# Kernel tuning notes

Measured on AMD Instinct MI355X. Metric: run time of the kernel, lower is better.

The kernel has to match this reference:

```python
import jax, jax.numpy as jnp
import numpy as np

B, S, D = 4, 4096, 256

def setup_inputs() -> dict:
    key = jax.random.key(0)
    kx, kq, kk, kv = jax.random.split(key, 4)
    # torch nn.Linear(D, D) weight init: U(-1/sqrt(D), 1/sqrt(D)), stored as [out, in]
    bound = 1.0 / np.sqrt(D)
    x = jax.random.normal(kx, (B, S, D), dtype=jnp.float32)
    Wq = jax.random.uniform(kq, (D, D), dtype=jnp.float32, minval=-bound, maxval=bound)
    Wk = jax.random.uniform(kk, (D, D), dtype=jnp.float32, minval=-bound, maxval=bound)
    Wv = jax.random.uniform(kv, (D, D), dtype=jnp.float32, minval=-bound, maxval=bound)
    return {"x": x, "Wq": Wq, "Wk": Wk, "Wv": Wv}

def reference(x, Wq, Wk, Wv):
    # Linear with weight [out,in]: y = x @ W^T
    Q = jnp.einsum('bsd,ed->bse', x, Wq)
    K = jnp.einsum('bsd,ed->bse', x, Wk)
    V = jnp.einsum('bsd,ed->bse', x, Wv)
    d = x.shape[-1]
    scores = jnp.einsum('bqe,bke->bqk', Q, K) / jnp.sqrt(jnp.float32(d))  # [B,S,S]
    S_len = x.shape[1]
    causal = jnp.tril(jnp.ones((S_len, S_len), dtype=bool))
    scores = jnp.where(causal, scores, -jnp.inf)
    attn = jax.nn.softmax(scores, axis=-1)
    return jnp.einsum('bqk,bke->bqe', attn, V)
```

## Files before the change

### kernel.cpp

```cpp
#include <hip/hip_runtime.h>

typedef unsigned short u16;
typedef unsigned int u32;
typedef __attribute__((ext_vector_type(8))) short bf16x8;
typedef __attribute__((ext_vector_type(4))) float f32x4;
typedef __attribute__((ext_vector_type(16))) float f32x16;
typedef __attribute__((ext_vector_type(2))) unsigned int u32x2;

#define MFMA16 __builtin_amdgcn_mfma_f32_16x16x32_bf16
#define MFMA32 __builtin_amdgcn_mfma_f32_32x32x16_bf16

__device__ __forceinline__ u16 f2bf(float f) {
  u32 u = __builtin_bit_cast(u32, f);
  u = u + 0x7FFFu + ((u >> 16) & 1u);
  return (u16)(u >> 16);
}
__device__ __forceinline__ u32 pk2(float lo, float hi) {
  return (u32)f2bf(lo) | ((u32)f2bf(hi) << 16);
}
__device__ __forceinline__ float bf2f(u32 x) {
  return __builtin_bit_cast(float, x << 16);
}
__device__ __forceinline__ u32 cvtpk(float lo, float hi) {
  u32 r;
  asm("v_cvt_pk_bf16_f32 %0, %1, %2" : "=v"(r) : "v"(lo), "v"(hi));
  return r;
}
__device__ __forceinline__ void pswap(u32& x, u32& y) {
  asm("v_permlane32_swap_b32 %0, %1" : "+v"(x), "+v"(y));
}
__device__ __forceinline__ void gld16(const void* gp, void* lp) {
  __builtin_amdgcn_global_load_lds((const __attribute__((address_space(1))) u32*)gp,
                                   (__attribute__((address_space(3))) u32*)lp, 16, 0, 0);
}

__global__ __launch_bounds__(256) void cvt_kernel(
    const float* __restrict__ x, const float* __restrict__ wq,
    const float* __restrict__ wk, const float* __restrict__ wv,
    u16* __restrict__ xbf, u16* __restrict__ wbf) {
  int idx = blockIdx.x * 256 + threadIdx.x;
  if (idx < 1048576) {
    float4 v = ((const float4*)x)[idx];
    uint2 u; u.x = pk2(v.x, v.y); u.y = pk2(v.z, v.w);
    ((uint2*)xbf)[idx] = u;
  } else {
    int j = idx - 1048576;
    const float* W = (j < 16384) ? wq : (j < 32768) ? wk : wv;
    int k = j & 16383;
    float4 v = ((const float4*)W)[k];
    uint2 u; u.x = pk2(v.x, v.y); u.y = pk2(v.z, v.w);
    ((uint2*)wbf)[j] = u;
  }
}

__global__ __launch_bounds__(256, 2) void proj_kernel(
    const u16* __restrict__ xbf, const u16* __restrict__ wbf,
    u16* __restrict__ Qs, u16* __restrict__ Ks, u16* __restrict__ Vt) {
  int tile = blockIdx.x, mat = blockIdx.y;
  int tid = threadIdx.x, w = tid >> 6, lane = tid & 63, b15 = lane & 15, g = lane >> 4;
  int base = tile * 64 + w * 16;
  const u16* W = wbf + mat * 65536;
  const u16* Xp = xbf + (size_t)(base + b15) * 256;
  f32x4 acc[16] = {};
  if (mat < 2) {
#pragma unroll
    for (int kk = 0; kk < 8; ++kk) {
      bf16x8 xf = *(const bf16x8*)(Xp + kk * 32 + g * 8);
#pragma unroll
      for (int eb = 0; eb < 16; ++eb) {
        bf16x8 wf = *(const bf16x8*)(W + (size_t)(eb * 16 + b15) * 256 + kk * 32 + g * 8);
        acc[eb] = MFMA16(xf, wf, acc[eb], 0, 0, 0);
      }
    }
    float scale = (mat == 0) ? 0.0901684400555602f : 1.0f;
    u16* dst = (mat == 0) ? Qs : Ks;
#pragma unroll
    for (int eb = 0; eb < 16; ++eb)
#pragma unroll
      for (int r = 0; r < 4; ++r)
        dst[(size_t)(base + g * 4 + r) * 256 + eb * 16 + b15] = f2bf(acc[eb][r] * scale);
  } else {
#pragma unroll
    for (int kk = 0; kk < 8; ++kk) {
      bf16x8 xf = *(const bf16x8*)(Xp + kk * 32 + g * 8);
#pragma unroll
      for (int eb = 0; eb < 16; ++eb) {
        bf16x8 wf = *(const bf16x8*)(W + (size_t)(eb * 16 + b15) * 256 + kk * 32 + g * 8);
        acc[eb] = MFMA16(wf, xf, acc[eb], 0, 0, 0);
      }
    }
    int sglob = base + b15;
    int b = sglob >> 12, sl = sglob & 4095;
#pragma unroll
    for (int eb = 0; eb < 16; ++eb)
#pragma unroll
      for (int r = 0; r < 4; ++r) {
        int e = eb * 16 + g * 4 + r;
        Vt[((size_t)(b * 256 + e) << 12) + sl] = f2bf(acc[eb][r]);
      }
  }
}

__global__ __launch_bounds__(256, 2) void attn_kernel(
    const u16* __restrict__ Qs, const u16* __restrict__ Ks_,
    const u16* __restrict__ Vt_, u16* __restrict__ pacc, float2* __restrict__ pml) {
  __shared__ u16 Kd[2][8192];
  __shared__ u16 Vd[2][8192];

  int bid = blockIdx.x;
  int xcd = bid & 7;
  int b = xcd >> 1;
  int j = ((bid >> 3) << 1) | (bid & 1);
  int t0, c0, t1 = -1, c1 = 0;
  if (j < 16) {
    int g = j & 7;
    if (j < 8) { t0 = 4 * g;     t1 = 4 * g + 3; }
    else       { t0 = 4 * g + 1; t1 = 4 * g + 2; }
    c0 = g; c1 = g;
  } else {
    int jj = j - 16;
    int g = 1;
#pragma unroll
    for (int gg = 2; gg <= 7; ++gg) if (jj >= 2 * gg * (gg - 1)) g = gg;
    int r = jj - 2 * g * (g - 1);
    t0 = 4 * g + r / g; c0 = r % g;
  }

  int tid = threadIdx.x, w = tid >> 6, lane = tid & 63;
  int l31 = lane & 31, h = lane >> 5;

  int Koff[4], Voff[4];
#pragma unroll
  for (int i = 0; i < 4; ++i) {
    int o = (w * 4 + i) * 1024 + lane * 16;
    int row = o >> 9;
    Koff[i] = row * 512 + ((o & 511) ^ ((row & 15) << 4));
    int e = o >> 6;
    Voff[i] = e * 8192 + ((o & 63) ^ (((e >> 1) & 3) << 4));
  }
  const char* Kgb = (const char*)(Ks_ + (size_t)b * 4096 * 256);
  const char* Vgb = (const char*)(Vt_ + (size_t)b * 1048576);
  char* KL = (char*)&Kd[0][0];
  char* VL = (char*)&Vd[0][0];

  auto stage = [&](int buf, int kt) {
    size_t kb = (size_t)kt * 32 * 512;
    size_t vb = (size_t)kt * 64;
#pragma unroll
    for (int i = 0; i < 4; ++i)
      gld16(Kgb + kb + Koff[i], KL + buf * 16384 + (w * 4 + i) * 1024);
#pragma unroll
    for (int i = 0; i < 4; ++i)
      gld16(Vgb + vb + Voff[i], VL + buf * 16384 + (w * 4 + i) * 1024);
  };

  auto process = [&](int tt, int c) {
    int g4 = tt >> 2;
    int uid = b * 144 + 2 * g4 * (g4 + 1) + (tt & 3) * (g4 + 1) + c;
    int qbase = tt * 128 + w * 32;
    int qrow = qbase + l31;
    int kt0 = 16 * c, kt_end = min(16 * c + 16, 4 * (tt + 1));

    const u16* Qrow = Qs + ((size_t)b * 4096 + qrow) * 256;
    bf16x8 qf[16];
#pragma unroll
    for (int kc = 0; kc < 16; ++kc)
      qf[kc] = *(const bf16x8*)(Qrow + kc * 16 + h * 8);

    f32x16 acc[8] = {};
    float m0 = -3e38f, l0 = 0.f;
    stage(0, kt0);
    int cur = 0;

    for (int kt = kt0; kt < kt_end; ++kt) {
      __syncthreads();
      if (kt + 1 < kt_end) stage(cur ^ 1, kt + 1);
      int kv0 = kt * 32;
      if (kv0 <= qbase + 31) {
        const char* Kc = KL + cur * 16384;
        const char* Vc = VL + cur * 16384;
        f32x16 sA = {}, sB = {};
        __builtin_amdgcn_s_setprio(1);
#pragma unroll
        for (int kc = 0; kc < 16; kc += 2) {
          bf16x8 k0 = *(const bf16x8*)(Kc + l31 * 512 + ((kc * 32 + h * 16) ^ ((l31 & 15) << 4)));
          bf16x8 k1 = *(const bf16x8*)(Kc + l31 * 512 + (((kc + 1) * 32 + h * 16) ^ ((l31 & 15) << 4)));
          sA = MFMA32(k0, qf[kc], sA, 0, 0, 0);
          sB = MFMA32(k1, qf[kc + 1], sB, 0, 0, 0);
        }
        __builtin_amdgcn_s_setprio(0);
        f32x16 s = sA + sB;
        if (kv0 + 31 > qbase) {
#pragma unroll
          for (int r = 0; r < 16; ++r) {
            int kv = kv0 + (r & 3) + 8 * (r >> 2) + 4 * h;
            if (kv > qrow) s[r] = -3e38f;
          }
        }
        float a0 = fmaxf(fmaxf(s[0], s[1]), s[2]);
        float a1 = fmaxf(fmaxf(s[3], s[4]), s[5]);
        float a2 = fmaxf(fmaxf(s[6], s[7]), s[8]);
        float a3 = fmaxf(fmaxf(s[9], s[10]), s[11]);
        float a4 = fmaxf(fmaxf(s[12], s[13]), s[14]);
        float pmh = fmaxf(fmaxf(fmaxf(a0, a1), fmaxf(a2, a3)), fmaxf(a4, s[15]));
        if (__any(pmh > m0 + 8.f)) {
          float pm = fmaxf(pmh, __shfl_xor(pmh, 32));
          float mn = fmaxf(m0, pm);
          float sc = exp2f(m0 - mn);
          l0 *= sc;
#pragma unroll
          for (int et = 0; et < 8; ++et) acc[et] *= sc;
          m0 = mn;
        }
        float p[16];
#pragma unroll
        for (int r = 0; r < 16; ++r) p[r] = exp2f(s[r] - m0);
        u32 w0 = cvtpk(p[0], p[1]),   w1 = cvtpk(p[2], p[3]);
        u32 w2 = cvtpk(p[4], p[5]),   w3 = cvtpk(p[6], p[7]);
        u32 w4 = cvtpk(p[8], p[9]),   w5 = cvtpk(p[10], p[11]);
        u32 w6 = cvtpk(p[12], p[13]), w7 = cvtpk(p[14], p[15]);
        pswap(w0, w2); pswap(w1, w3);
        pswap(w4, w6); pswap(w5, w7);
        union { u32 uu[4]; bf16x8 vv; } pA, pB;
        pA.uu[0] = w0; pA.uu[1] = w1; pA.uu[2] = w2; pA.uu[3] = w3;
        pB.uu[0] = w4; pB.uu[1] = w5; pB.uu[2] = w6; pB.uu[3] = w7;
        __builtin_amdgcn_s_setprio(1);
#pragma unroll
        for (int et = 0; et < 8; ++et) {
          const char* vrow = Vc + (et * 32 + l31) * 64;
          int swz = ((l31 >> 1) & 3) << 4;
          bf16x8 vf0 = *(const bf16x8*)(vrow + ((h * 16) ^ swz));
          bf16x8 vf1 = *(const bf16x8*)(vrow + ((32 + h * 16) ^ swz));
          acc[et] = MFMA32(vf0, pA.vv, acc[et], 0, 0, 0);
          acc[et] = MFMA32(vf1, pB.vv, acc[et], 0, 0, 0);
        }
        __builtin_amdgcn_s_setprio(0);
        float q0 = (p[0] + p[1]) + (p[2] + p[3]);
        float q1 = (p[4] + p[5]) + (p[6] + p[7]);
        float q2 = (p[8] + p[9]) + (p[10] + p[11]);
        float q3 = (p[12] + p[13]) + (p[14] + p[15]);
        l0 += (q0 + q1) + (q2 + q3);
      }
      cur ^= 1;
    }

    l0 += __shfl_xor(l0, 32);

    u16* ppr = pacc + ((size_t)uid * 128 + w * 32 + l31) * 256;
#pragma unroll
    for (int et = 0; et < 8; ++et)
#pragma unroll
      for (int jj = 0; jj < 4; ++jj) {
        u32x2 o;
        o[0] = pk2(acc[et][4 * jj], acc[et][4 * jj + 1]);
        o[1] = pk2(acc[et][4 * jj + 2], acc[et][4 * jj + 3]);
        *(u32x2*)(ppr + et * 32 + 8 * jj + 4 * h) = o;
      }
    if (h == 0) {
      float2 a; a.x = m0; a.y = l0;
      pml[(size_t)uid * 128 + w * 32 + l31] = a;
    }
  };

  process(t0, c0);
  if (t1 >= 0) {
    __syncthreads();
    process(t1, c1);
  }
}

__global__ __launch_bounds__(256) void combine_kernel(
    const u16* __restrict__ pacc, const float2* __restrict__ pml,
    float* __restrict__ out) {
  int row = blockIdx.x * 4 + (threadIdx.x >> 6);
  int lane = threadIdx.x & 63;
  int b = row >> 12, r = row & 4095;
  int tt = r >> 7, rin = r & 127;
  int g4 = tt >> 2, nch = g4 + 1;
  int ubase = b * 144 + 2 * g4 * (g4 + 1) + (tt & 3) * (g4 + 1);
  float M = -3e38f;
  for (int cc = 0; cc < nch; ++cc)
    M = fmaxf(M, pml[(size_t)(ubase + cc) * 128 + rin].x);
  float L = 0.f, o0 = 0.f, o1 = 0.f, o2 = 0.f, o3 = 0.f;
  for (int cc = 0; cc < nch; ++cc) {
    float2 ml = pml[(size_t)(ubase + cc) * 128 + rin];
    float s = exp2f(ml.x - M);
    L += ml.y * s;
    u32x2 a = *(const u32x2*)(pacc + ((size_t)(ubase + cc) * 128 + rin) * 256 + lane * 4);
    o0 += s * bf2f(a[0] & 0xffffu); o1 += s * bf2f(a[0] >> 16);
    o2 += s * bf2f(a[1] & 0xffffu); o3 += s * bf2f(a[1] >> 16);
  }
  float inv = 1.f / L;
  f32x4 res = {o0 * inv, o1 * inv, o2 * inv, o3 * inv};
  *(f32x4*)(out + (size_t)row * 256 + lane * 4) = res;
}

extern "C" void kernel_launch(void* const* d_in, const int* in_sizes, int n_in,
                              void* d_out, int out_size, void* d_ws, size_t ws_size,
                              hipStream_t stream) {
  const float* x = (const float*)d_in[0];
  const float* wq = (const float*)d_in[1];
  const float* wk = (const float*)d_in[2];
  const float* wv = (const float*)d_in[3];
  char* ws = (char*)d_ws;
  u16* xbf = (u16*)(ws);
  u16* wbf = (u16*)(ws + 8388608);
  u16* Qs  = (u16*)(ws + 9437184);
  u16* Ks  = (u16*)(ws + 17825792);
  u16* Vt  = (u16*)(ws + 26214400);
  u16* pacc = (u16*)(ws + 34603008);
  float2* pml = (float2*)(ws + 72351744);
  float* out = (float*)d_out;

  hipLaunchKernelGGL(cvt_kernel, dim3(4288), dim3(256), 0, stream, x, wq, wk, wv, xbf, wbf);
  hipLaunchKernelGGL(proj_kernel, dim3(256, 3), dim3(256), 0, stream, xbf, wbf, Qs, Ks, Vt);
  hipLaunchKernelGGL(attn_kernel, dim3(512), dim3(256), 0, stream, Qs, Ks, Vt, pacc, pml);
  hipLaunchKernelGGL(combine_kernel, dim3(4096), dim3(256), 0, stream, pacc, pml, out);
}
```

Baseline: 158.5 us.

## Fuse x conversion into projection and combine into attention via last-block reduction

The separate fp32-to-bf16 conversion of x is removed: the projection kernel now loads fp32 x and converts it in registers. The combine kernel is folded into the attention kernel. Single-chunk tiles write normalized output directly, and multi-chunk tiles use an atomic counter so the last finishing block merges the partials. This saves a kernel launch and the bf16 x round trip through memory, at the cost of three-fold redundant x loads and conversion in projection and serialized combine work at the tail of some attention blocks.

```diff
diff --git a/kernel.cpp b/kernel.cpp
--- a/kernel.cpp
+++ b/kernel.cpp
@@ -35,43 +35,49 @@
 }
 
 __global__ __launch_bounds__(256) void cvt_kernel(
-    const float* __restrict__ x, const float* __restrict__ wq,
-    const float* __restrict__ wk, const float* __restrict__ wv,
-    u16* __restrict__ xbf, u16* __restrict__ wbf) {
+    const float* __restrict__ wq, const float* __restrict__ wk,
+    const float* __restrict__ wv, u16* __restrict__ wbf, u32* __restrict__ cnt) {
   int idx = blockIdx.x * 256 + threadIdx.x;
-  if (idx < 1048576) {
-    float4 v = ((const float4*)x)[idx];
-    uint2 u; u.x = pk2(v.x, v.y); u.y = pk2(v.z, v.w);
-    ((uint2*)xbf)[idx] = u;
-  } else {
-    int j = idx - 1048576;
-    const float* W = (j < 16384) ? wq : (j < 32768) ? wk : wv;
-    int k = j & 16383;
-    float4 v = ((const float4*)W)[k];
-    uint2 u; u.x = pk2(v.x, v.y); u.y = pk2(v.z, v.w);
-    ((uint2*)wbf)[j] = u;
-  }
+  const float* W = (idx < 16384) ? wq : (idx < 32768) ? wk : wv;
+  int k = idx & 16383;
+  float4 v = ((const float4*)W)[k];
+  uint2 u; u.x = pk2(v.x, v.y); u.y = pk2(v.z, v.w);
+  ((uint2*)wbf)[idx] = u;
+  if (blockIdx.x == 0 && threadIdx.x < 128) cnt[threadIdx.x] = 0;
 }
 
 __global__ __launch_bounds__(256, 2) void proj_kernel(
-    const u16* __restrict__ xbf, const u16* __restrict__ wbf,
+    const float* __restrict__ x, const u16* __restrict__ wbf,
     u16* __restrict__ Qs, u16* __restrict__ Ks, u16* __restrict__ Vt) {
   int tile = blockIdx.x, mat = blockIdx.y;
   int tid = threadIdx.x, w = tid >> 6, lane = tid & 63, b15 = lane & 15, g = lane >> 4;
   int base = tile * 64 + w * 16;
   const u16* W = wbf + mat * 65536;
-  const u16* Xp = xbf + (size_t)(base + b15) * 256;
+  const float* Xp = x + (size_t)(base + b15) * 256;
   f32x4 acc[16] = {};
-  if (mat < 2) {
-#pragma unroll
-    for (int kk = 0; kk < 8; ++kk) {
-      bf16x8 xf = *(const bf16x8*)(Xp + kk * 32 + g * 8);
+#pragma unroll
+  for (int kk = 0; kk < 8; ++kk) {
+    float4 xa = *(const float4*)(Xp + kk * 32 + g * 8);
+    float4 xb = *(const float4*)(Xp + kk * 32 + g * 8 + 4);
+    union { u32 u[4]; bf16x8 v; } xu;
+    xu.u[0] = cvtpk(xa.x, xa.y); xu.u[1] = cvtpk(xa.z, xa.w);
+    xu.u[2] = cvtpk(xb.x, xb.y); xu.u[3] = cvtpk(xb.z, xb.w);
+    bf16x8 xf = xu.v;
+    if (mat < 2) {
 #pragma unroll
       for (int eb = 0; eb < 16; ++eb) {
         bf16x8 wf = *(const bf16x8*)(W + (size_t)(eb * 16 + b15) * 256 + kk * 32 + g * 8);
         acc[eb] = MFMA16(xf, wf, acc[eb], 0, 0, 0);
       }
-    }
+    } else {
+#pragma unroll
+      for (int eb = 0; eb < 16; ++eb) {
+        bf16x8 wf = *(const bf16x8*)(W + (size_t)(eb * 16 + b15) * 256 + kk * 32 + g * 8);
+        acc[eb] = MFMA16(wf, xf, acc[eb], 0, 0, 0);
+      }
+    }
+  }
+  if (mat < 2) {
     float scale = (mat == 0) ? 0.0901684400555602f : 1.0f;
     u16* dst = (mat == 0) ? Qs : Ks;
 #pragma unroll
@@ -80,15 +86,6 @@
       for (int r = 0; r < 4; ++r)
         dst[(size_t)(base + g * 4 + r) * 256 + eb * 16 + b15] = f2bf(acc[eb][r] * scale);
   } else {
-#pragma unroll
-    for (int kk = 0; kk < 8; ++kk) {
-      bf16x8 xf = *(const bf16x8*)(Xp + kk * 32 + g * 8);
-#pragma unroll
-      for (int eb = 0; eb < 16; ++eb) {
-        bf16x8 wf = *(const bf16x8*)(W + (size_t)(eb * 16 + b15) * 256 + kk * 32 + g * 8);
-        acc[eb] = MFMA16(wf, xf, acc[eb], 0, 0, 0);
-      }
-    }
     int sglob = base + b15;
     int b = sglob >> 12, sl = sglob & 4095;
 #pragma unroll
@@ -103,9 +100,11 @@
 
 __global__ __launch_bounds__(256, 2) void attn_kernel(
     const u16* __restrict__ Qs, const u16* __restrict__ Ks_,
-    const u16* __restrict__ Vt_, u16* __restrict__ pacc, float2* __restrict__ pml) {
+    const u16* __restrict__ Vt_, u16* __restrict__ pacc, float2* __restrict__ pml,
+    float* __restrict__ outp, u32* __restrict__ cnt) {
   __shared__ u16 Kd[2][8192];
   __shared__ u16 Vd[2][8192];
+  __shared__ int lastFlag;
 
   int bid = blockIdx.x;
   int xcd = bid & 7;
@@ -156,7 +155,9 @@
 
   auto process = [&](int tt, int c) {
     int g4 = tt >> 2;
-    int uid = b * 144 + 2 * g4 * (g4 + 1) + (tt & 3) * (g4 + 1) + c;
+    int nch = g4 + 1;
+    int ubase = b * 144 + 2 * g4 * (g4 + 1) + (tt & 3) * nch;
+    int uid = ubase + c;
     int qbase = tt * 128 + w * 32;
     int qrow = qbase + l31;
     int kt0 = 16 * c, kt_end = min(16 * c + 16, 4 * (tt + 1));
@@ -246,6 +247,20 @@
 
     l0 += __shfl_xor(l0, 32);
 
+    if (nch == 1) {
+      float inv = 1.f / l0;
+      float* Op = outp + ((size_t)(b * 4096) + qrow) * 256;
+#pragma unroll
+      for (int et = 0; et < 8; ++et)
+#pragma unroll
+        for (int jj = 0; jj < 4; ++jj) {
+          f32x4 res = {acc[et][4 * jj] * inv, acc[et][4 * jj + 1] * inv,
+                       acc[et][4 * jj + 2] * inv, acc[et][4 * jj + 3] * inv};
+          *(f32x4*)(Op + et * 32 + 8 * jj + 4 * h) = res;
+        }
+      return;
+    }
+
     u16* ppr = pacc + ((size_t)uid * 128 + w * 32 + l31) * 256;
 #pragma unroll
     for (int et = 0; et < 8; ++et)
@@ -260,6 +275,35 @@
       float2 a; a.x = m0; a.y = l0;
       pml[(size_t)uid * 128 + w * 32 + l31] = a;
     }
+
+    __threadfence();
+    __syncthreads();
+    if (tid == 0) {
+      u32 old = atomicAdd(&cnt[b * 32 + tt], 1u);
+      lastFlag = (old == (u32)(nch - 1)) ? 1 : 0;
+    }
+    __syncthreads();
+    if (lastFlag) {
+      __threadfence();
+      int rg = tid >> 6, ln = tid & 63;
+      for (int rr = rg; rr < 128; rr += 4) {
+        float M = -3e38f;
+        for (int cc = 0; cc < nch; ++cc)
+          M = fmaxf(M, pml[(size_t)(ubase + cc) * 128 + rr].x);
+        float L = 0.f, o0 = 0.f, o1 = 0.f, o2 = 0.f, o3 = 0.f;
+        for (int cc = 0; cc < nch; ++cc) {
+          float2 ml = pml[(size_t)(ubase + cc) * 128 + rr];
+          float sfac = exp2f(ml.x - M);
+          L += ml.y * sfac;
+          u32x2 a = *(const u32x2*)(pacc + ((size_t)(ubase + cc) * 128 + rr) * 256 + ln * 4);
+          o0 += sfac * bf2f(a[0] & 0xffffu); o1 += sfac * bf2f(a[0] >> 16);
+          o2 += sfac * bf2f(a[1] & 0xffffu); o3 += sfac * bf2f(a[1] >> 16);
+        }
+        float inv = 1.f / L;
+        f32x4 res = {o0 * inv, o1 * inv, o2 * inv, o3 * inv};
+        *(f32x4*)(outp + ((size_t)(b * 4096 + tt * 128 + rr)) * 256 + ln * 4) = res;
+      }
+    }
   };
 
   process(t0, c0);
@@ -267,32 +311,6 @@
     __syncthreads();
     process(t1, c1);
   }
-}
-
-__global__ __launch_bounds__(256) void combine_kernel(
-    const u16* __restrict__ pacc, const float2* __restrict__ pml,
-    float* __restrict__ out) {
-  int row = blockIdx.x * 4 + (threadIdx.x >> 6);
-  int lane = threadIdx.x & 63;
-  int b = row >> 12, r = row & 4095;
-  int tt = r >> 7, rin = r & 127;
-  int g4 = tt >> 2, nch = g4 + 1;
-  int ubase = b * 144 + 2 * g4 * (g4 + 1) + (tt & 3) * (g4 + 1);
-  float M = -3e38f;
-  for (int cc = 0; cc < nch; ++cc)
-    M = fmaxf(M, pml[(size_t)(ubase + cc) * 128 + rin].x);
-  float L = 0.f, o0 = 0.f, o1 = 0.f, o2 = 0.f, o3 = 0.f;
-  for (int cc = 0; cc < nch; ++cc) {
-    float2 ml = pml[(size_t)(ubase + cc) * 128 + rin];
-    float s = exp2f(ml.x - M);
-    L += ml.y * s;
-    u32x2 a = *(const u32x2*)(pacc + ((size_t)(ubase + cc) * 128 + rin) * 256 + lane * 4);
-    o0 += s * bf2f(a[0] & 0xffffu); o1 += s * bf2f(a[0] >> 16);
-    o2 += s * bf2f(a[1] & 0xffffu); o3 += s * bf2f(a[1] >> 16);
-  }
-  float inv = 1.f / L;
-  f32x4 res = {o0 * inv, o1 * inv, o2 * inv, o3 * inv};
-  *(f32x4*)(out + (size_t)row * 256 + lane * 4) = res;
 }
 
 extern "C" void kernel_launch(void* const* d_in, const int* in_sizes, int n_in,
@@ -303,17 +321,16 @@
   const float* wk = (const float*)d_in[2];
   const float* wv = (const float*)d_in[3];
   char* ws = (char*)d_ws;
-  u16* xbf = (u16*)(ws);
-  u16* wbf = (u16*)(ws + 8388608);
-  u16* Qs  = (u16*)(ws + 9437184);
-  u16* Ks  = (u16*)(ws + 17825792);
-  u16* Vt  = (u16*)(ws + 26214400);
-  u16* pacc = (u16*)(ws + 34603008);
-  float2* pml = (float2*)(ws + 72351744);
+  u16* wbf = (u16*)(ws);
+  u16* Qs  = (u16*)(ws + 1048576);
+  u16* Ks  = (u16*)(ws + 9437184);
+  u16* Vt  = (u16*)(ws + 17825792);
+  u16* pacc = (u16*)(ws + 26214400);
+  float2* pml = (float2*)(ws + 63963136);
+  u32* cnt = (u32*)(ws + 64552960);
   float* out = (float*)d_out;
 
-  hipLaunchKernelGGL(cvt_kernel, dim3(4288), dim3(256), 0, stream, x, wq, wk, wv, xbf, wbf);
-  hipLaunchKernelGGL(proj_kernel, dim3(256, 3), dim3(256), 0, stream, xbf, wbf, Qs, Ks, Vt);
-  hipLaunchKernelGGL(attn_kernel, dim3(512), dim3(256), 0, stream, Qs, Ks, Vt, pacc, pml);
-  hipLaunchKernelGGL(combine_kernel, dim3(4096), dim3(256), 0, stream, pacc, pml, out);
-}
+  hipLaunchKernelGGL(cvt_kernel, dim3(192), dim3(256), 0, stream, wq, wk, wv, wbf, cnt);
+  hipLaunchKernelGGL(proj_kernel, dim3(256, 3), dim3(256), 0, stream, x, wbf, Qs, Ks, Vt);
+  hipLaunchKernelGGL(attn_kernel, dim3(512), dim3(256), 0, stream, Qs, Ks, Vt, pacc, pml, out, cnt);
+}
```

Result: slower. 371.8 us (+134.5%).

## Load K and V fragments directly from global memory instead of LDS staging

Applied to the files above, without the earlier changes.

Removes the double-buffered LDS staging of K and V tiles (global_load_lds plus barriers) in the attention kernel. Each wave now reads its K rows and transposed V fragments straight from global memory into registers before the MFMAs. This drops the __syncthreads and the shared-memory footprint, but each of the four waves now fetches the same K/V data separately. Global load latency is also no longer hidden by prefetching the next tile.

```diff
diff --git a/kernel.cpp b/kernel.cpp
--- a/kernel.cpp
+++ b/kernel.cpp
@@ -28,10 +28,6 @@
 }
 __device__ __forceinline__ void pswap(u32& x, u32& y) {
   asm("v_permlane32_swap_b32 %0, %1" : "+v"(x), "+v"(y));
-}
-__device__ __forceinline__ void gld16(const void* gp, void* lp) {
-  __builtin_amdgcn_global_load_lds((const __attribute__((address_space(1))) u32*)gp,
-                                   (__attribute__((address_space(3))) u32*)lp, 16, 0, 0);
 }
 
 __global__ __launch_bounds__(256) void cvt_kernel(
@@ -104,9 +100,6 @@
 __global__ __launch_bounds__(256, 2) void attn_kernel(
     const u16* __restrict__ Qs, const u16* __restrict__ Ks_,
     const u16* __restrict__ Vt_, u16* __restrict__ pacc, float2* __restrict__ pml) {
-  __shared__ u16 Kd[2][8192];
-  __shared__ u16 Vd[2][8192];
-
   int bid = blockIdx.x;
   int xcd = bid & 7;
   int b = xcd >> 1;
@@ -129,30 +122,8 @@
   int tid = threadIdx.x, w = tid >> 6, lane = tid & 63;
   int l31 = lane & 31, h = lane >> 5;
 
-  int Koff[4], Voff[4];
-#pragma unroll
-  for (int i = 0; i < 4; ++i) {
-    int o = (w * 4 + i) * 1024 + lane * 16;
-    int row = o >> 9;
-    Koff[i] = row * 512 + ((o & 511) ^ ((row & 15) << 4));
-    int e = o >> 6;
-    Voff[i] = e * 8192 + ((o & 63) ^ (((e >> 1) & 3) << 4));
-  }
-  const char* Kgb = (const char*)(Ks_ + (size_t)b * 4096 * 256);
-  const char* Vgb = (const char*)(Vt_ + (size_t)b * 1048576);
-  char* KL = (char*)&Kd[0][0];
-  char* VL = (char*)&Vd[0][0];
-
-  auto stage = [&](int buf, int kt) {
-    size_t kb = (size_t)kt * 32 * 512;
-    size_t vb = (size_t)kt * 64;
-#pragma unroll
-    for (int i = 0; i < 4; ++i)
-      gld16(Kgb + kb + Koff[i], KL + buf * 16384 + (w * 4 + i) * 1024);
-#pragma unroll
-    for (int i = 0; i < 4; ++i)
-      gld16(Vgb + vb + Voff[i], VL + buf * 16384 + (w * 4 + i) * 1024);
-  };
+  const u16* Kgb = Ks_ + (size_t)b * 4096 * 256;
+  const u16* Vgb = Vt_ + (size_t)b * 1048576;
 
   auto process = [&](int tt, int c) {
     int g4 = tt >> 2;
@@ -169,79 +140,72 @@
 
     f32x16 acc[8] = {};
     float m0 = -3e38f, l0 = 0.f;
-    stage(0, kt0);
-    int cur = 0;
 
     for (int kt = kt0; kt < kt_end; ++kt) {
-      __syncthreads();
-      if (kt + 1 < kt_end) stage(cur ^ 1, kt + 1);
       int kv0 = kt * 32;
-      if (kv0 <= qbase + 31) {
-        const char* Kc = KL + cur * 16384;
-        const char* Vc = VL + cur * 16384;
-        f32x16 sA = {}, sB = {};
-        __builtin_amdgcn_s_setprio(1);
-#pragma unroll
-        for (int kc = 0; kc < 16; kc += 2) {
-          bf16x8 k0 = *(const bf16x8*)(Kc + l31 * 512 + ((kc * 32 + h * 16) ^ ((l31 & 15) << 4)));
-          bf16x8 k1 = *(const bf16x8*)(Kc + l31 * 512 + (((kc + 1) * 32 + h * 16) ^ ((l31 & 15) << 4)));
-          sA = MFMA32(k0, qf[kc], sA, 0, 0, 0);
-          sB = MFMA32(k1, qf[kc + 1], sB, 0, 0, 0);
+      if (kv0 > qbase + 31) continue;
+      const u16* Kp = Kgb + (size_t)(kv0 + l31) * 256 + h * 8;
+      f32x16 sA = {}, sB = {};
+      __builtin_amdgcn_s_setprio(1);
+#pragma unroll
+      for (int kc = 0; kc < 16; kc += 2) {
+        bf16x8 k0 = *(const bf16x8*)(Kp + kc * 16);
+        bf16x8 k1 = *(const bf16x8*)(Kp + (kc + 1) * 16);
+        sA = MFMA32(k0, qf[kc], sA, 0, 0, 0);
+        sB = MFMA32(k1, qf[kc + 1], sB, 0, 0, 0);
+      }
+      __builtin_amdgcn_s_setprio(0);
+      f32x16 s = sA + sB;
+      if (kv0 + 31 > qbase) {
+#pragma unroll
+        for (int r = 0; r < 16; ++r) {
+          int kv = kv0 + (r & 3) + 8 * (r >> 2) + 4 * h;
+          if (kv > qrow) s[r] = -3e38f;
         }
-        __builtin_amdgcn_s_setprio(0);
-        f32x16 s = sA + sB;
-        if (kv0 + 31 > qbase) {
-#pragma unroll
-          for (int r = 0; r < 16; ++r) {
-            int kv = kv0 + (r & 3) + 8 * (r >> 2) + 4 * h;
-            if (kv > qrow) s[r] = -3e38f;
-          }
-        }
-        float a0 = fmaxf(fmaxf(s[0], s[1]), s[2]);
-        float a1 = fmaxf(fmaxf(s[3], s[4]), s[5]);
-        float a2 = fmaxf(fmaxf(s[6], s[7]), s[8]);
-        float a3 = fmaxf(fmaxf(s[9], s[10]), s[11]);
-        float a4 = fmaxf(fmaxf(s[12], s[13]), s[14]);
-        float pmh = fmaxf(fmaxf(fmaxf(a0, a1), fmaxf(a2, a3)), fmaxf(a4, s[15]));
-        if (__any(pmh > m0 + 8.f)) {
-          float pm = fmaxf(pmh, __shfl_xor(pmh, 32));
-          float mn = fmaxf(m0, pm);
-          float sc = exp2f(m0 - mn);
-          l0 *= sc;
-#pragma unroll
-          for (int et = 0; et < 8; ++et) acc[et] *= sc;
-          m0 = mn;
-        }
-        float p[16];
-#pragma unroll
-        for (int r = 0; r < 16; ++r) p[r] = exp2f(s[r] - m0);
-        u32 w0 = cvtpk(p[0], p[1]),   w1 = cvtpk(p[2], p[3]);
-        u32 w2 = cvtpk(p[4], p[5]),   w3 = cvtpk(p[6], p[7]);
-        u32 w4 = cvtpk(p[8], p[9]),   w5 = cvtpk(p[10], p[11]);
-        u32 w6 = cvtpk(p[12], p[13]), w7 = cvtpk(p[14], p[15]);
-        pswap(w0, w2); pswap(w1, w3);
-        pswap(w4, w6); pswap(w5, w7);
-        union { u32 uu[4]; bf16x8 vv; } pA, pB;
-        pA.uu[0] = w0; pA.uu[1] = w1; pA.uu[2] = w2; pA.uu[3] = w3;
-        pB.uu[0] = w4; pB.uu[1] = w5; pB.uu[2] = w6; pB.uu[3] = w7;
-        __builtin_amdgcn_s_setprio(1);
-#pragma unroll
-        for (int et = 0; et < 8; ++et) {
-          const char* vrow = Vc + (et * 32 + l31) * 64;
-          int swz = ((l31 >> 1) & 3) << 4;
-          bf16x8 vf0 = *(const bf16x8*)(vrow + ((h * 16) ^ swz));
-          bf16x8 vf1 = *(const bf16x8*)(vrow + ((32 + h * 16) ^ swz));
-          acc[et] = MFMA32(vf0, pA.vv, acc[et], 0, 0, 0);
-          acc[et] = MFMA32(vf1, pB.vv, acc[et], 0, 0, 0);
-        }
-        __builtin_amdgcn_s_setprio(0);
-        float q0 = (p[0] + p[1]) + (p[2] + p[3]);
-        float q1 = (p[4] + p[5]) + (p[6] + p[7]);
-        float q2 = (p[8] + p[9]) + (p[10] + p[11]);
-        float q3 = (p[12] + p[13]) + (p[14] + p[15]);
-        l0 += (q0 + q1) + (q2 + q3);
-      }
-      cur ^= 1;
+      }
+      float a0 = fmaxf(fmaxf(s[0], s[1]), s[2]);
+      float a1 = fmaxf(fmaxf(s[3], s[4]), s[5]);
+      float a2 = fmaxf(fmaxf(s[6], s[7]), s[8]);
+      float a3 = fmaxf(fmaxf(s[9], s[10]), s[11]);
+      float a4 = fmaxf(fmaxf(s[12], s[13]), s[14]);
+      float pmh = fmaxf(fmaxf(fmaxf(a0, a1), fmaxf(a2, a3)), fmaxf(a4, s[15]));
+      if (__any(pmh > m0 + 8.f)) {
+        float pm = fmaxf(pmh, __shfl_xor(pmh, 32));
+        float mn = fmaxf(m0, pm);
+        float sc = exp2f(m0 - mn);
+        l0 *= sc;
+#pragma unroll
+        for (int et = 0; et < 8; ++et) acc[et] *= sc;
+        m0 = mn;
+      }
+      float p[16];
+#pragma unroll
+      for (int r = 0; r < 16; ++r) p[r] = exp2f(s[r] - m0);
+      u32 w0 = cvtpk(p[0], p[1]),   w1 = cvtpk(p[2], p[3]);
+      u32 w2 = cvtpk(p[4], p[5]),   w3 = cvtpk(p[6], p[7]);
+      u32 w4 = cvtpk(p[8], p[9]),   w5 = cvtpk(p[10], p[11]);
+      u32 w6 = cvtpk(p[12], p[13]), w7 = cvtpk(p[14], p[15]);
+      pswap(w0, w2); pswap(w1, w3);
+      pswap(w4, w6); pswap(w5, w7);
+      union { u32 uu[4]; bf16x8 vv; } pA, pB;
+      pA.uu[0] = w0; pA.uu[1] = w1; pA.uu[2] = w2; pA.uu[3] = w3;
+      pB.uu[0] = w4; pB.uu[1] = w5; pB.uu[2] = w6; pB.uu[3] = w7;
+      const u16* Vp = Vgb + (size_t)l31 * 4096 + kv0 + h * 8;
+      __builtin_amdgcn_s_setprio(1);
+#pragma unroll
+      for (int et = 0; et < 8; ++et) {
+        bf16x8 vf0 = *(const bf16x8*)(Vp);
+        bf16x8 vf1 = *(const bf16x8*)(Vp + 16);
+        acc[et] = MFMA32(vf0, pA.vv, acc[et], 0, 0, 0);
+        acc[et] = MFMA32(vf1, pB.vv, acc[et], 0, 0, 0);
+        Vp += 32 * 4096;
+      }
+      __builtin_amdgcn_s_setprio(0);
+      float q0 = (p[0] + p[1]) + (p[2] + p[3]);
+      float q1 = (p[4] + p[5]) + (p[6] + p[7]);
+      float q2 = (p[8] + p[9]) + (p[10] + p[11]);
+      float q3 = (p[12] + p[13]) + (p[14] + p[15]);
+      l0 += (q0 + q1) + (q2 + q3);
     }
 
     l0 += __shfl_xor(l0, 32);
@@ -263,10 +227,7 @@
   };
 
   process(t0, c0);
-  if (t1 >= 0) {
-    __syncthreads();
-    process(t1, c1);
-  }
+  if (t1 >= 0) process(t1, c1);
 }
 
 __global__ __launch_bounds__(256) void combine_kernel(
```

New measurement: 216.6 us. +36.6%, slower.
